# Kernel tuning notes

Measured on AMD Instinct MI355X. Metric: run time of the kernel, lower is better.

Reference implementation:

```python
import jax, jax.numpy as jnp
import numpy as np

B, H, W, C = 32, 64, 64, 256


def setup_inputs() -> dict:
    key = jax.random.key(0)
    kq, kk, kv = jax.random.split(key, 3)
    query = jax.random.normal(kq, (B, H, W, C), dtype=jnp.float32)
    keys = jax.random.normal(kk, (B, H, W, C), dtype=jnp.float32)
    values = jax.random.normal(kv, (B, H, W, C), dtype=jnp.float32)
    return {"query": query, "keys": keys, "values": values}


def reference(query, keys, values):
    # A[b,q,k] = sum_{h,w} query[b,h,w,q] * keys[b,h,w,k]
    scores = jnp.einsum("bhwq,bhwk->bqk", query, keys)
    attn = jax.nn.softmax(scores, axis=-1)  # softmax over keys axis
    # out[b,q,h,w] = sum_k attn[b,q,k] * values[b,h,w,k]
    out = jnp.einsum("bqk,bhwk->bqhw", attn, values)
    return out
```

## Files before the change

kernel.cpp:

```cpp
#include <hip/hip_runtime.h>
#include <hip/hip_bf16.h>

#define B_  32
#define HW_ 4096
#define C_  256
#define S_LDS 40

using bf16x8 = __attribute__((ext_vector_type(8))) short;
using f32x4  = __attribute__((ext_vector_type(4))) float;

__device__ __forceinline__ ushort f2bf_rn(float x) {
    uint u = __builtin_bit_cast(uint, x);
    u += 0x7FFFu + ((u >> 16) & 1u);
    return (ushort)(u >> 16);
}
__device__ __forceinline__ uint pk_bf2(float a, float b) {
    return ((uint)f2bf_rn(b) << 16) | (uint)f2bf_rn(a);
}
__device__ __forceinline__ uint pk_rtz(float x0, float x1) {
    return __builtin_amdgcn_perm(__builtin_bit_cast(uint, x1),
                                 __builtin_bit_cast(uint, x0), 0x07060302u);
}
__device__ __forceinline__ void split2_rtz(float x0, float x1, uint& hi2, uint& lo2) {
    uint u0 = __builtin_bit_cast(uint, x0), u1 = __builtin_bit_cast(uint, x1);
    hi2 = __builtin_amdgcn_perm(u1, u0, 0x07060302u);
    float h0 = __builtin_bit_cast(float, u0 & 0xFFFF0000u);
    float h1 = __builtin_bit_cast(float, u1 & 0xFFFF0000u);
    lo2 = pk_rtz(x0 - h0, x1 - h1);
}

__global__ __launch_bounds__(512, 4) void scores_kernel(const float* __restrict__ qg,
                                                        const float* __restrict__ kg,
                                                        float* __restrict__ scores) {
    int x  = blockIdx.x;
    int s  = x & 3;
    int tn = (x >> 2) & 1;
    int tm = (x >> 3) & 1;
    int b  = x >> 4;

    __shared__ __align__(16) ushort Qhi[128 * S_LDS], Qlo[128 * S_LDS];
    __shared__ __align__(16) ushort Khi[128 * S_LDS], Klo[128 * S_LDS];

    int tid = threadIdx.x, lane = tid & 63, w = tid >> 6;
    int m0 = (w >> 2) * 64;
    int n0 = (w & 3) * 32;
    int g = lane >> 4, r16 = lane & 15;

    int cc = tid & 127;
    int hh = (tid >> 7) * 8;

    const float* qcol = qg + (size_t)b * HW_ * C_ + tm * 128 + cc;
    const float* kcol = kg + (size_t)b * HW_ * C_ + tn * 128 + cc;

    f32x4 acc[4][2];
#pragma unroll
    for (int i = 0; i < 4; ++i)
#pragma unroll
        for (int j = 0; j < 2; ++j) acc[i][j] = (f32x4){0.f, 0.f, 0.f, 0.f};

#define LOAD_QK(qr, kr, itv) {                                                 \
        int hw0 = s * 1024 + (itv) * 32 + hh;                                  \
        const float* qp = qcol + (size_t)hw0 * C_;                             \
        const float* kp = kcol + (size_t)hw0 * C_;                             \
        _Pragma("unroll")                                                      \
        for (int j = 0; j < 8; ++j) qr[j] = qp[(size_t)j * C_];                \
        _Pragma("unroll")                                                      \
        for (int j = 0; j < 8; ++j) kr[j] = kp[(size_t)j * C_];                \
    }

#define CONVERT_STORE(qr, kr) {                                                \
        uint qh[4], ql[4], kh[4], kl[4];                                       \
        _Pragma("unroll")                                                      \
        for (int p = 0; p < 4; ++p) {                                          \
            split2_rtz(qr[2*p], qr[2*p+1], qh[p], ql[p]);                      \
            split2_rtz(kr[2*p], kr[2*p+1], kh[p], kl[p]);                      \
        }                                                                      \
        int base_ = cc * S_LDS + hh;                                           \
        *reinterpret_cast<uint4*>(&Qhi[base_]) = make_uint4(qh[0], qh[1], qh[2], qh[3]); \
        *reinterpret_cast<uint4*>(&Qlo[base_]) = make_uint4(ql[0], ql[1], ql[2], ql[3]); \
        *reinterpret_cast<uint4*>(&Khi[base_]) = make_uint4(kh[0], kh[1], kh[2], kh[3]); \
        *reinterpret_cast<uint4*>(&Klo[base_]) = make_uint4(kl[0], kl[1], kl[2], kl[3]); \
    }

#define MFMA_PHASE() {                                                         \
        bf16x8 ahi[4], alo[4];                                                 \
        _Pragma("unroll")                                                      \
        for (int mi = 0; mi < 4; ++mi) {                                       \
            int off = (m0 + mi * 16 + r16) * S_LDS + g * 8;                    \
            ahi[mi] = *reinterpret_cast<const bf16x8*>(&Qhi[off]);             \
            alo[mi] = *reinterpret_cast<const bf16x8*>(&Qlo[off]);             \
        }                                                                      \
        _Pragma("unroll")                                                      \
        for (int ni = 0; ni < 2; ++ni) {                                       \
            int off = (n0 + ni * 16 + r16) * S_LDS + g * 8;                    \
            bf16x8 bhi = *reinterpret_cast<const bf16x8*>(&Khi[off]);          \
            bf16x8 blo = *reinterpret_cast<const bf16x8*>(&Klo[off]);          \
            _Pragma("unroll")                                                  \
            for (int mi = 0; mi < 4; ++mi) {                                   \
                acc[mi][ni] = __builtin_amdgcn_mfma_f32_16x16x32_bf16(ahi[mi], bhi, acc[mi][ni], 0, 0, 0); \
                acc[mi][ni] = __builtin_amdgcn_mfma_f32_16x16x32_bf16(ahi[mi], blo, acc[mi][ni], 0, 0, 0); \
                acc[mi][ni] = __builtin_amdgcn_mfma_f32_16x16x32_bf16(alo[mi], bhi, acc[mi][ni], 0, 0, 0); \
            }                                                                  \
        }                                                                      \
    }

#define STEP(qc, kc, qn, kn, itv, doload) {                                    \
        if (doload) LOAD_QK(qn, kn, (itv) + 1);                                \
        __syncthreads();                                                       \
        CONVERT_STORE(qc, kc);                                                 \
        __syncthreads();                                                       \
        MFMA_PHASE();                                                          \
    }

    float qa[8], ka[8], qb[8], kb[8];
    LOAD_QK(qa, ka, 0);
    for (int p = 0; p < 16; ++p) {
        STEP(qa, ka, qb, kb, 2 * p, true);
        STEP(qb, kb, qa, ka, 2 * p + 1, p < 15);
    }

#pragma unroll
    for (int mi = 0; mi < 4; ++mi)
#pragma unroll
        for (int ni = 0; ni < 2; ++ni)
#pragma unroll
            for (int r = 0; r < 4; ++r) {
                int qrow = tm * 128 + m0 + mi * 16 + g * 4 + r;
                int kc   = tn * 128 + n0 + ni * 16 + r16;
                atomicAdd(&scores[((size_t)b * 256 + qrow) * 256 + kc], acc[mi][ni][r]);
            }
#undef STEP
#undef MFMA_PHASE
#undef CONVERT_STORE
#undef LOAD_QK
}

__global__ __launch_bounds__(256) void softmax_kernel(const float* __restrict__ scores,
                                                      ushort* __restrict__ attn) {
    int wid  = blockIdx.x * 4 + (threadIdx.x >> 6);
    int lane = threadIdx.x & 63;
    const float4 v = *reinterpret_cast<const float4*>(scores + (size_t)wid * 256 + lane * 4);
    float m = fmaxf(fmaxf(v.x, v.y), fmaxf(v.z, v.w));
#pragma unroll
    for (int off = 32; off; off >>= 1) m = fmaxf(m, __shfl_xor(m, off, 64));
    float e0 = __expf(v.x - m), e1 = __expf(v.y - m), e2 = __expf(v.z - m), e3 = __expf(v.w - m);
    float ssum = e0 + e1 + e2 + e3;
#pragma unroll
    for (int off = 32; off; off >>= 1) ssum += __shfl_xor(ssum, off, 64);
    float inv = 1.0f / ssum;
    uint2 o;
    o.x = pk_bf2(e0 * inv, e1 * inv);
    o.y = pk_bf2(e2 * inv, e3 * inv);
    *reinterpret_cast<uint2*>(attn + (size_t)wid * 256 + lane * 4) = o;
}

__global__ __launch_bounds__(256, 3) void pv_kernel(const ushort* __restrict__ attn,
                                                    const float* __restrict__ vg,
                                                    float* __restrict__ out) {
    int b   = blockIdx.x >> 6;
    int hw0 = (blockIdx.x & 63) * 64;
    int tid = threadIdx.x, lane = tid & 63, w = tid >> 6;
    int m0  = w * 64;
    int g   = lane >> 4, r16 = lane & 15;

    const ushort* abase = attn + (size_t)b * 256 * 256 + g * 8;
    const float*  vbase = vg + ((size_t)(b * HW_ + hw0 + r16)) * C_ + g * 8;

    f32x4 acc[4][4];
#pragma unroll
    for (int i = 0; i < 4; ++i)
#pragma unroll
        for (int j = 0; j < 4; ++j) acc[i][j] = (f32x4){0.f, 0.f, 0.f, 0.f};

#define K3_LOAD(abuf, vbuf, ksv) {                                             \
        int k0_ = (ksv) * 32;                                                  \
        _Pragma("unroll")                                                      \
        for (int mi = 0; mi < 4; ++mi)                                         \
            abuf[mi] = *reinterpret_cast<const bf16x8*>(abase + (size_t)(m0 + mi * 16 + r16) * 256 + k0_); \
        _Pragma("unroll")                                                      \
        for (int ni = 0; ni < 4; ++ni) {                                       \
            const float* vp_ = vbase + (size_t)ni * 16 * C_ + k0_;             \
            vbuf[ni][0] = *reinterpret_cast<const float4*>(vp_);               \
            vbuf[ni][1] = *reinterpret_cast<const float4*>(vp_ + 4);           \
        }                                                                      \
    }

#define K3_COMPUTE(abuf, vbuf) {                                               \
        _Pragma("unroll")                                                      \
        for (int ni = 0; ni < 4; ++ni) {                                       \
            bf16x8 bf;                                                         \
            uint* bu = reinterpret_cast<uint*>(&bf);                           \
            bu[0] = pk_rtz(vbuf[ni][0].x, vbuf[ni][0].y);                      \
            bu[1] = pk_rtz(vbuf[ni][0].z, vbuf[ni][0].w);                      \
            bu[2] = pk_rtz(vbuf[ni][1].x, vbuf[ni][1].y);                      \
            bu[3] = pk_rtz(vbuf[ni][1].z, vbuf[ni][1].w);                      \
            _Pragma("unroll")                                                  \
            for (int mi = 0; mi < 4; ++mi)                                     \
                acc[mi][ni] = __builtin_amdgcn_mfma_f32_16x16x32_bf16(abuf[mi], bf, acc[mi][ni], 0, 0, 0); \
        }                                                                      \
    }

    bf16x8 aA[4], aB[4];
    float4 vA[4][2], vB[4][2];
    K3_LOAD(aA, vA, 0);
#pragma unroll
    for (int p = 0; p < 4; ++p) {
        K3_LOAD(aB, vB, 2 * p + 1);
        K3_COMPUTE(aA, vA);
        if (p < 3) K3_LOAD(aA, vA, 2 * p + 2);
        K3_COMPUTE(aB, vB);
    }
#undef K3_LOAD
#undef K3_COMPUTE

#pragma unroll
    for (int mi = 0; mi < 4; ++mi)
#pragma unroll
        for (int ni = 0; ni < 4; ++ni)
#pragma unroll
            for (int r = 0; r < 4; ++r) {
                int qrow = m0 + mi * 16 + g * 4 + r;
                int hw   = hw0 + ni * 16 + r16;
                out[((size_t)b * 256 + qrow) * 4096 + hw] = acc[mi][ni][r];
            }
}

extern "C" void kernel_launch(void* const* d_in, const int* in_sizes, int n_in,
                              void* d_out, int out_size, void* d_ws, size_t ws_size,
                              hipStream_t stream) {
    const float* q = (const float*)d_in[0];
    const float* k = (const float*)d_in[1];
    const float* v = (const float*)d_in[2];
    float* out = (float*)d_out;

    float*  scores = (float*)d_ws;
    ushort* attn   = (ushort*)((char*)d_ws + (size_t)B_ * 256 * 256 * 4);

    (void)hipMemsetAsync(d_ws, 0, (size_t)B_ * 256 * 256 * 4, stream);
    scores_kernel<<<512, 512, 0, stream>>>(q, k, scores);
    softmax_kernel<<<2048, 256, 0, stream>>>(scores, attn);
    pv_kernel<<<2048, 256, 0, stream>>>(attn, v, out);
}
```

Before: 215.4 us.

## Stage raw fp32 tiles in swizzled LDS and split scores reduction further

The scores kernel now stores raw fp32 Q/K tiles in XOR-swizzled shared memory and does the bf16 hi/lo split after reading fragments, instead of pre-converting into padded bf16 arrays. Its HW reduction is split 8 ways instead of 4, doubling the grid to add parallelism at the cost of more atomics. The PV kernel now stages V through a double-buffered swizzled LDS tile with coalesced row loads instead of strided per-lane global loads, and its occupancy hint rises to 4. The conversion work in the scores kernel is repeated per fragment read rather than once per element.

```diff
diff --git a/kernel.cpp b/kernel.cpp
--- a/kernel.cpp
+++ b/kernel.cpp
@@ -4,10 +4,10 @@
 #define B_  32
 #define HW_ 4096
 #define C_  256
-#define S_LDS 40
 
 using bf16x8 = __attribute__((ext_vector_type(8))) short;
 using f32x4  = __attribute__((ext_vector_type(4))) float;
+using u32x4  = __attribute__((ext_vector_type(4))) uint;
 
 __device__ __forceinline__ ushort f2bf_rn(float x) {
     uint u = __builtin_bit_cast(uint, x);
@@ -28,18 +28,27 @@
     float h1 = __builtin_bit_cast(float, u1 & 0xFFFF0000u);
     lo2 = pk_rtz(x0 - h0, x1 - h1);
 }
+__device__ __forceinline__ void frag_from_f32(const f32x4& f0, const f32x4& f1,
+                                              bf16x8& hi, bf16x8& lo) {
+    uint h0, l0, h1, l1, h2, l2, h3, l3;
+    split2_rtz(f0[0], f0[1], h0, l0);
+    split2_rtz(f0[2], f0[3], h1, l1);
+    split2_rtz(f1[0], f1[1], h2, l2);
+    split2_rtz(f1[2], f1[3], h3, l3);
+    hi = __builtin_bit_cast(bf16x8, (u32x4){h0, h1, h2, h3});
+    lo = __builtin_bit_cast(bf16x8, (u32x4){l0, l1, l2, l3});
+}
 
 __global__ __launch_bounds__(512, 4) void scores_kernel(const float* __restrict__ qg,
                                                         const float* __restrict__ kg,
                                                         float* __restrict__ scores) {
     int x  = blockIdx.x;
-    int s  = x & 3;
-    int tn = (x >> 2) & 1;
-    int tm = (x >> 3) & 1;
-    int b  = x >> 4;
-
-    __shared__ __align__(16) ushort Qhi[128 * S_LDS], Qlo[128 * S_LDS];
-    __shared__ __align__(16) ushort Khi[128 * S_LDS], Klo[128 * S_LDS];
+    int s  = x & 7;
+    int tn = (x >> 3) & 1;
+    int tm = (x >> 4) & 1;
+    int b  = x >> 5;
+
+    __shared__ __align__(16) float Qt[128 * 32], Kt[128 * 32];
 
     int tid = threadIdx.x, lane = tid & 63, w = tid >> 6;
     int m0 = (w >> 2) * 64;
@@ -47,7 +56,11 @@
     int g = lane >> 4, r16 = lane & 15;
 
     int cc = tid & 127;
-    int hh = (tid >> 7) * 8;
+    int s0 = (tid >> 7) * 2;
+    int hh = s0 * 4;
+
+    int wi0 = cc * 32 + ((s0 ^ (cc & 7)) * 4);
+    int wi1 = cc * 32 + (((s0 + 1) ^ (cc & 7)) * 4);
 
     const float* qcol = qg + (size_t)b * HW_ * C_ + tm * 128 + cc;
     const float* kcol = kg + (size_t)b * HW_ * C_ + tn * 128 + cc;
@@ -59,7 +72,7 @@
         for (int j = 0; j < 2; ++j) acc[i][j] = (f32x4){0.f, 0.f, 0.f, 0.f};
 
 #define LOAD_QK(qr, kr, itv) {                                                 \
-        int hw0 = s * 1024 + (itv) * 32 + hh;                                  \
+        int hw0 = s * 512 + (itv) * 32 + hh;                                   \
         const float* qp = qcol + (size_t)hw0 * C_;                             \
         const float* kp = kcol + (size_t)hw0 * C_;                             \
         _Pragma("unroll")                                                      \
@@ -68,33 +81,29 @@
         for (int j = 0; j < 8; ++j) kr[j] = kp[(size_t)j * C_];                \
     }
 
-#define CONVERT_STORE(qr, kr) {                                                \
-        uint qh[4], ql[4], kh[4], kl[4];                                       \
-        _Pragma("unroll")                                                      \
-        for (int p = 0; p < 4; ++p) {                                          \
-            split2_rtz(qr[2*p], qr[2*p+1], qh[p], ql[p]);                      \
-            split2_rtz(kr[2*p], kr[2*p+1], kh[p], kl[p]);                      \
-        }                                                                      \
-        int base_ = cc * S_LDS + hh;                                           \
-        *reinterpret_cast<uint4*>(&Qhi[base_]) = make_uint4(qh[0], qh[1], qh[2], qh[3]); \
-        *reinterpret_cast<uint4*>(&Qlo[base_]) = make_uint4(ql[0], ql[1], ql[2], ql[3]); \
-        *reinterpret_cast<uint4*>(&Khi[base_]) = make_uint4(kh[0], kh[1], kh[2], kh[3]); \
-        *reinterpret_cast<uint4*>(&Klo[base_]) = make_uint4(kl[0], kl[1], kl[2], kl[3]); \
+#define STORE_RAW(qr, kr) {                                                    \
+        *reinterpret_cast<f32x4*>(&Qt[wi0]) = (f32x4){qr[0], qr[1], qr[2], qr[3]}; \
+        *reinterpret_cast<f32x4*>(&Qt[wi1]) = (f32x4){qr[4], qr[5], qr[6], qr[7]}; \
+        *reinterpret_cast<f32x4*>(&Kt[wi0]) = (f32x4){kr[0], kr[1], kr[2], kr[3]}; \
+        *reinterpret_cast<f32x4*>(&Kt[wi1]) = (f32x4){kr[4], kr[5], kr[6], kr[7]}; \
     }
 
 #define MFMA_PHASE() {                                                         \
         bf16x8 ahi[4], alo[4];                                                 \
         _Pragma("unroll")                                                      \
         for (int mi = 0; mi < 4; ++mi) {                                       \
-            int off = (m0 + mi * 16 + r16) * S_LDS + g * 8;                    \
-            ahi[mi] = *reinterpret_cast<const bf16x8*>(&Qhi[off]);             \
-            alo[mi] = *reinterpret_cast<const bf16x8*>(&Qlo[off]);             \
+            int row = m0 + mi * 16 + r16, key = row & 7;                       \
+            f32x4 f0 = *reinterpret_cast<const f32x4*>(&Qt[row * 32 + (((2*g)   ^ key) * 4)]); \
+            f32x4 f1 = *reinterpret_cast<const f32x4*>(&Qt[row * 32 + (((2*g+1) ^ key) * 4)]); \
+            frag_from_f32(f0, f1, ahi[mi], alo[mi]);                           \
         }                                                                      \
         _Pragma("unroll")                                                      \
         for (int ni = 0; ni < 2; ++ni) {                                       \
-            int off = (n0 + ni * 16 + r16) * S_LDS + g * 8;                    \
-            bf16x8 bhi = *reinterpret_cast<const bf16x8*>(&Khi[off]);          \
-            bf16x8 blo = *reinterpret_cast<const bf16x8*>(&Klo[off]);          \
+            int row = n0 + ni * 16 + r16, key = row & 7;                       \
+            f32x4 f0 = *reinterpret_cast<const f32x4*>(&Kt[row * 32 + (((2*g)   ^ key) * 4)]); \
+            f32x4 f1 = *reinterpret_cast<const f32x4*>(&Kt[row * 32 + (((2*g+1) ^ key) * 4)]); \
+            bf16x8 bhi, blo;                                                   \
+            frag_from_f32(f0, f1, bhi, blo);                                   \
             _Pragma("unroll")                                                  \
             for (int mi = 0; mi < 4; ++mi) {                                   \
                 acc[mi][ni] = __builtin_amdgcn_mfma_f32_16x16x32_bf16(ahi[mi], bhi, acc[mi][ni], 0, 0, 0); \
@@ -107,16 +116,16 @@
 #define STEP(qc, kc, qn, kn, itv, doload) {                                    \
         if (doload) LOAD_QK(qn, kn, (itv) + 1);                                \
         __syncthreads();                                                       \
-        CONVERT_STORE(qc, kc);                                                 \
+        STORE_RAW(qc, kc);                                                     \
         __syncthreads();                                                       \
         MFMA_PHASE();                                                          \
     }
 
     float qa[8], ka[8], qb[8], kb[8];
     LOAD_QK(qa, ka, 0);
-    for (int p = 0; p < 16; ++p) {
+    for (int p = 0; p < 8; ++p) {
         STEP(qa, ka, qb, kb, 2 * p, true);
-        STEP(qb, kb, qa, ka, 2 * p + 1, p < 15);
+        STEP(qb, kb, qa, ka, 2 * p + 1, p < 7);
     }
 
 #pragma unroll
@@ -131,7 +140,7 @@
             }
 #undef STEP
 #undef MFMA_PHASE
-#undef CONVERT_STORE
+#undef STORE_RAW
 #undef LOAD_QK
 }
 
@@ -154,7 +163,7 @@
     *reinterpret_cast<uint2*>(attn + (size_t)wid * 256 + lane * 4) = o;
 }
 
-__global__ __launch_bounds__(256, 3) void pv_kernel(const ushort* __restrict__ attn,
+__global__ __launch_bounds__(256, 4) void pv_kernel(const ushort* __restrict__ attn,
                                                     const float* __restrict__ vg,
                                                     float* __restrict__ out) {
     int b   = blockIdx.x >> 6;
@@ -163,8 +172,15 @@
     int m0  = w * 64;
     int g   = lane >> 4, r16 = lane & 15;
 
+    __shared__ __align__(16) float Vt[2 * 64 * 32];
+
+    int srow = tid >> 2;
+    int sslot = (tid & 3) * 2;
+    int wi0 = srow * 32 + ((sslot ^ (srow & 7)) * 4);
+    int wi1 = srow * 32 + (((sslot + 1) ^ (srow & 7)) * 4);
+    const float* vstage = vg + ((size_t)(b * HW_ + hw0 + srow)) * C_ + sslot * 4;
+
     const ushort* abase = attn + (size_t)b * 256 * 256 + g * 8;
-    const float*  vbase = vg + ((size_t)(b * HW_ + hw0 + r16)) * C_ + g * 8;
 
     f32x4 acc[4][4];
 #pragma unroll
@@ -172,46 +188,49 @@
 #pragma unroll
         for (int j = 0; j < 4; ++j) acc[i][j] = (f32x4){0.f, 0.f, 0.f, 0.f};
 
-#define K3_LOAD(abuf, vbuf, ksv) {                                             \
-        int k0_ = (ksv) * 32;                                                  \
-        _Pragma("unroll")                                                      \
-        for (int mi = 0; mi < 4; ++mi)                                         \
-            abuf[mi] = *reinterpret_cast<const bf16x8*>(abase + (size_t)(m0 + mi * 16 + r16) * 256 + k0_); \
-        _Pragma("unroll")                                                      \
-        for (int ni = 0; ni < 4; ++ni) {                                       \
-            const float* vp_ = vbase + (size_t)ni * 16 * C_ + k0_;             \
-            vbuf[ni][0] = *reinterpret_cast<const float4*>(vp_);               \
-            vbuf[ni][1] = *reinterpret_cast<const float4*>(vp_ + 4);           \
-        }                                                                      \
-    }
-
-#define K3_COMPUTE(abuf, vbuf) {                                               \
-        _Pragma("unroll")                                                      \
-        for (int ni = 0; ni < 4; ++ni) {                                       \
-            bf16x8 bf;                                                         \
-            uint* bu = reinterpret_cast<uint*>(&bf);                           \
-            bu[0] = pk_rtz(vbuf[ni][0].x, vbuf[ni][0].y);                      \
-            bu[1] = pk_rtz(vbuf[ni][0].z, vbuf[ni][0].w);                      \
-            bu[2] = pk_rtz(vbuf[ni][1].x, vbuf[ni][1].y);                      \
-            bu[3] = pk_rtz(vbuf[ni][1].z, vbuf[ni][1].w);                      \
-            _Pragma("unroll")                                                  \
-            for (int mi = 0; mi < 4; ++mi)                                     \
-                acc[mi][ni] = __builtin_amdgcn_mfma_f32_16x16x32_bf16(abuf[mi], bf, acc[mi][ni], 0, 0, 0); \
-        }                                                                      \
-    }
-
-    bf16x8 aA[4], aB[4];
-    float4 vA[4][2], vB[4][2];
-    K3_LOAD(aA, vA, 0);
-#pragma unroll
-    for (int p = 0; p < 4; ++p) {
-        K3_LOAD(aB, vB, 2 * p + 1);
-        K3_COMPUTE(aA, vA);
-        if (p < 3) K3_LOAD(aA, vA, 2 * p + 2);
-        K3_COMPUTE(aB, vB);
-    }
-#undef K3_LOAD
-#undef K3_COMPUTE
+    {
+        f32x4 p0 = *reinterpret_cast<const f32x4*>(vstage);
+        f32x4 p1 = *reinterpret_cast<const f32x4*>(vstage + 4);
+        *reinterpret_cast<f32x4*>(&Vt[wi0]) = p0;
+        *reinterpret_cast<f32x4*>(&Vt[wi1]) = p1;
+    }
+    __syncthreads();
+
+    for (int p = 0; p < 8; ++p) {
+        float* rbuf = &Vt[(p & 1) * 64 * 32];
+        float* wbuf = &Vt[((p + 1) & 1) * 64 * 32];
+
+        f32x4 n0v, n1v;
+        if (p < 7) {
+            n0v = *reinterpret_cast<const f32x4*>(vstage + (p + 1) * 32);
+            n1v = *reinterpret_cast<const f32x4*>(vstage + (p + 1) * 32 + 4);
+        }
+
+        int k0 = p * 32;
+        bf16x8 a[4];
+#pragma unroll
+        for (int mi = 0; mi < 4; ++mi)
+            a[mi] = *reinterpret_cast<const bf16x8*>(abase + (size_t)(m0 + mi * 16 + r16) * 256 + k0);
+
+#pragma unroll
+        for (int ni = 0; ni < 4; ++ni) {
+            int row = ni * 16 + r16, key = row & 7;
+            f32x4 f0 = *reinterpret_cast<const f32x4*>(&rbuf[row * 32 + (((2 * g)     ^ key) * 4)]);
+            f32x4 f1 = *reinterpret_cast<const f32x4*>(&rbuf[row * 32 + (((2 * g + 1) ^ key) * 4)]);
+            bf16x8 bf = __builtin_bit_cast(bf16x8, (u32x4){
+                pk_rtz(f0[0], f0[1]), pk_rtz(f0[2], f0[3]),
+                pk_rtz(f1[0], f1[1]), pk_rtz(f1[2], f1[3])});
+#pragma unroll
+            for (int mi = 0; mi < 4; ++mi)
+                acc[mi][ni] = __builtin_amdgcn_mfma_f32_16x16x32_bf16(a[mi], bf, acc[mi][ni], 0, 0, 0);
+        }
+
+        if (p < 7) {
+            *reinterpret_cast<f32x4*>(&wbuf[wi0]) = n0v;
+            *reinterpret_cast<f32x4*>(&wbuf[wi1]) = n1v;
+            __syncthreads();
+        }
+    }
 
 #pragma unroll
     for (int mi = 0; mi < 4; ++mi)
@@ -237,7 +256,7 @@
     ushort* attn   = (ushort*)((char*)d_ws + (size_t)B_ * 256 * 256 * 4);
 
     (void)hipMemsetAsync(d_ws, 0, (size_t)B_ * 256 * 256 * 4, stream);
-    scores_kernel<<<512, 512, 0, stream>>>(q, k, scores);
+    scores_kernel<<<1024, 512, 0, stream>>>(q, k, scores);
     softmax_kernel<<<2048, 256, 0, stream>>>(scores, attn);
     pv_kernel<<<2048, 256, 0, stream>>>(attn, v, out);
 }
```

Measured after the change: 185.9 us. -13.7%, faster.
